# Kernel optimization log

Hardware: AMD Instinct MI355X
Metric: run time of the kernel (lower is better)

## Reference

```python
import jax, jax.numpy as jnp
import numpy as np

D = 256      # hidden_dim
NH = 8       # num_heads
DH = D // NH # head_dim = 32
K = 5        # base_kernel -> NA3D kernel (5,5,5), causal on axis 0 (time)
EPS = 1e-6


def _axis_idx(L, k, causal):
    """Per-axis NATTEN neighbor indices [L, k] and validity mask [L, k]."""
    i = jnp.arange(L)
    o = jnp.arange(k)
    if causal:
        idx = i[:, None] - (k - 1) + o[None, :]   # last k positions incl. self
        mask = idx >= 0
        idx = jnp.clip(idx, 0, L - 1)
    else:
        start = jnp.clip(i - k // 2, 0, L - k)     # window shifts at borders
        idx = start[:, None] + o[None, :]
        mask = jnp.ones((L, k), dtype=bool)
    return idx, mask


def _rmsnorm(x, w):
    return x * jax.lax.rsqrt(jnp.mean(x * x, axis=-1, keepdims=True) + EPS) * w


def _na3d(x, wq, bq, wk, bk, wv, bv, wo, bo):
    # x: [B, T, H, W, D]; neighborhood attention, causal in T.
    B, T, H, W, Dm = x.shape
    q = (x @ wq + bq).reshape(B, T, H, W, NH, DH)
    k = (x @ wk + bk).reshape(B, T, H, W, NH, DH)
    v = (x @ wv + bv).reshape(B, T, H, W, NH, DH)

    tidx, tmask = _axis_idx(T, K, True)
    hidx, _ = _axis_idx(H, K, False)
    widx, _ = _axis_idx(W, K, False)

    # Gather neighbor windows: [B, T, H, W, K, K, K, NH, DH]
    ti = tidx[:, None, None, :, None, None]
    hi = hidx[None, :, None, None, :, None]
    wi = widx[None, None, :, None, None, :]
    kn = k[:, ti, hi, wi].reshape(B, T, H, W, K ** 3, NH, DH)
    vn = v[:, ti, hi, wi].reshape(B, T, H, W, K ** 3, NH, DH)

    # Validity mask (only causal time axis masks anything): [T, H, W, K^3]
    mask = jnp.broadcast_to(tmask[:, None, None, :, None, None],
                            (T, H, W, K, K, K)).reshape(T, H, W, K ** 3)

    logits = jnp.einsum('bthwnd,bthwmnd->bthwnm', q, kn) * (DH ** -0.5)
    logits = jnp.where(mask[None, :, :, :, None, :], logits, -jnp.inf)
    attn = jax.nn.softmax(logits, axis=-1)
    out = jnp.einsum('bthwnm,bthwmnd->bthwnd', attn, vn).reshape(B, T, H, W, Dm)
    return out @ wo + bo


def setup_inputs() -> dict:
    key = jax.random.key(0)
    ks = jax.random.split(key, 14)
    w = lambda k_, shape: jax.random.normal(k_, shape, jnp.float32) * 0.02
    return {
        'x': jax.random.normal(ks[0], (1, 8, 16, 16, D), jnp.float32),
        'norm1_w': jnp.ones((D,), jnp.float32),
        'norm2_w': jnp.ones((D,), jnp.float32),
        'wq': w(ks[1], (D, D)), 'bq': jnp.zeros((D,), jnp.float32),
        'wk': w(ks[2], (D, D)), 'bk': jnp.zeros((D,), jnp.float32),
        'wv': w(ks[3], (D, D)), 'bv': jnp.zeros((D,), jnp.float32),
        'wo': w(ks[4], (D, D)), 'bo': jnp.zeros((D,), jnp.float32),
        'w1': w(ks[5], (D, 4 * D)),
        'w2': w(ks[6], (D, 4 * D)),
        'w3': w(ks[7], (4 * D, D)),
    }


def reference(x, norm1_w, norm2_w, wq, bq, wk, bk, wv, bv, wo, bo, w1, w2, w3):
    # residual NA block
    h = x + _na3d(_rmsnorm(x, norm1_w), wq, bq, wk, bk, wv, bv, wo, bo)
    # residual SwiGLU FFN block
    y = _rmsnorm(h, norm2_w)
    h = h + (jax.nn.silu(y @ w1) * (y @ w2)) @ w3
    return h
```

## Files before the change

### kernel.cpp

```cpp
#include <hip/hip_runtime.h>
#include <hip/hip_bf16.h>

typedef __attribute__((ext_vector_type(8))) __bf16 bf16x8;
typedef __attribute__((ext_vector_type(4))) __bf16 bf16x4;
typedef __attribute__((ext_vector_type(4))) short shortx4;
typedef __attribute__((ext_vector_type(4))) float f32x4;

#define D    256
#define FF   1024
#define NTOK 2048

__device__ __forceinline__ float ldf(const void* p, int i, bool isf32){
  return isf32 ? ((const float*)p)[i] : (float)(((const __bf16*)p)[i]);
}

__device__ __forceinline__ f32x4 mfma16x16x16bf16(bf16x4 a, bf16x4 b, f32x4 c){
#if __has_builtin(__builtin_amdgcn_mfma_f32_16x16x16_bf16)
  return __builtin_amdgcn_mfma_f32_16x16x16_bf16(a, b, c, 0, 0, 0);
#elif __has_builtin(__builtin_amdgcn_mfma_f32_16x16x16bf16_1k)
  return __builtin_amdgcn_mfma_f32_16x16x16bf16_1k(__builtin_bit_cast(shortx4, a),
                                                   __builtin_bit_cast(shortx4, b), c, 0, 0, 0);
#else
  asm volatile("v_mfma_f32_16x16x16_bf16 %0, %1, %2, %0" : "+v"(c) : "v"(a), "v"(b));
  return c;
#endif
}

struct MiscArgs { const void* x; const void* vec[6]; };
struct TPArgs { const void* src[7]; };

__global__ __launch_bounds__(256) void prep_kernel(MiscArgs a, TPArgs ta,
                                                   float* __restrict__ X,
                                                   float* __restrict__ VEC,
                                                   __bf16* __restrict__ WT,
                                                   __bf16* __restrict__ XN,
                                                   const unsigned int* __restrict__ tagp){
  __shared__ float tl[32][33];
  __shared__ float red[4];
  bool isf32 = (*tagp == 0x3F800000u);
  int b = blockIdx.x, tid = threadIdx.x;

  if (b < 1024){
    const void* src; int Kd, Nd, dstOff, tk, tn;
    if (b < 256){
      int mat = b >> 6, t = b & 63;
      src = ta.src[mat]; Kd = 256; Nd = 256; dstOff = mat*65536;
      tk = t >> 3; tn = t & 7;
    } else if (b < 768){
      int mat = (b - 256) >> 8, t = (b - 256) & 255;
      src = ta.src[4 + mat]; Kd = 256; Nd = 1024; dstOff = 262144 + mat*262144;
      tk = t >> 5; tn = t & 31;
    } else {
      int t = b - 768;
      src = ta.src[6]; Kd = 1024; Nd = 256; dstOff = 786432;
      tk = t >> 3; tn = t & 7;
    }
    int tx = tid & 31, ty = tid >> 5;
    int k0 = tk*32, n0 = tn*32;
    #pragma unroll
    for (int i = 0; i < 4; i++){
      int kk = ty + i*8;
      tl[kk][tx] = ldf(src, (k0 + kk)*Nd + n0 + tx, isf32);
    }
    __syncthreads();
    #pragma unroll
    for (int i = 0; i < 4; i++){
      int nn = ty + i*8;
      WT[dstOff + (n0 + nn)*Kd + k0 + tx] = (__bf16)tl[tx][nn];
    }
  } else if (b < 3072){
    int tok = b - 1024;
    int idx = tok*D + tid;
    float xv = ldf(a.x, idx, isf32);
    X[idx] = xv;
    float s = xv*xv;
    #pragma unroll
    for (int d = 32; d > 0; d >>= 1) s += __shfl_xor(s, d, 64);
    if ((tid & 63) == 0) red[tid >> 6] = s;
    __syncthreads();
    float tot = red[0]+red[1]+red[2]+red[3];
    float w = ldf(a.vec[0], tid, isf32);
    XN[idx] = (__bf16)(xv * rsqrtf(tot*(1.0f/D) + 1e-6f) * w);
  } else {
    for (int i = tid; i < 1536; i += 256)
      VEC[i] = ldf(a.vec[i >> 8], i & 255, isf32);
  }
}

__global__ __launch_bounds__(256) void rmsnorm_kernel(const float* __restrict__ x,
                                                      const float* __restrict__ w,
                                                      __bf16* __restrict__ out){
  int tok = blockIdx.x, tid = threadIdx.x;
  int idx = tok*D + tid;
  float xv = x[idx];
  float s = xv*xv;
  #pragma unroll
  for (int d = 32; d > 0; d >>= 1) s += __shfl_xor(s, d, 64);
  __shared__ float red[4];
  if ((tid & 63) == 0) red[tid >> 6] = s;
  __syncthreads();
  float tot = red[0]+red[1]+red[2]+red[3];
  out[idx] = (__bf16)(xv * rsqrtf(tot*(1.0f/D) + 1e-6f) * w[tid]);
}

typedef __bf16 ldsrow[72];

__device__ __forceinline__ void gemm_core(const __bf16* __restrict__ A,
                                          const __bf16* __restrict__ B,
                                          int K, int m0, int n0,
                                          ldsrow* As, ldsrow* Bs,
                                          f32x4 acc[2][2]){
  int tid = threadIdx.x;
  int wave = tid >> 6, lane = tid & 63;
  int wrow = wave & 1, wcol = wave >> 1;
  int q = lane >> 4, ln = lane & 15;
  for (int k0 = 0; k0 < K; k0 += 64){
    #pragma unroll
    for (int j = 0; j < 2; j++){
      int c = j*256 + tid;
      int row = c >> 3, seg = c & 7;
      *(float4*)&As[row][seg*8] = *(const float4*)&A[(m0+row)*K + k0 + seg*8];
      *(float4*)&Bs[row][seg*8] = *(const float4*)&B[(n0+row)*K + k0 + seg*8];
    }
    __syncthreads();
    #pragma unroll
    for (int ks = 0; ks < 2; ks++){
      bf16x8 a0 = *(const bf16x8*)&As[wrow*32      + ln][ks*32 + q*8];
      bf16x8 a1 = *(const bf16x8*)&As[wrow*32 + 16 + ln][ks*32 + q*8];
      bf16x8 b0 = *(const bf16x8*)&Bs[wcol*32      + ln][ks*32 + q*8];
      bf16x8 b1 = *(const bf16x8*)&Bs[wcol*32 + 16 + ln][ks*32 + q*8];
      acc[0][0] = __builtin_amdgcn_mfma_f32_16x16x32_bf16(a0, b0, acc[0][0], 0, 0, 0);
      acc[0][1] = __builtin_amdgcn_mfma_f32_16x16x32_bf16(a0, b1, acc[0][1], 0, 0, 0);
      acc[1][0] = __builtin_amdgcn_mfma_f32_16x16x32_bf16(a1, b0, acc[1][0], 0, 0, 0);
      acc[1][1] = __builtin_amdgcn_mfma_f32_16x16x32_bf16(a1, b1, acc[1][1], 0, 0, 0);
    }
    __syncthreads();
  }
}

#define GEMM_PROLOGUE \
  int tid = threadIdx.x; \
  int wave = tid >> 6, lane = tid & 63; \
  int wrow = wave & 1, wcol = wave >> 1; \
  int q = lane >> 4, ln = lane & 15; \
  (void)tid; \
  f32x4 acc[2][2]; \
  acc[0][0] = (f32x4){0,0,0,0}; acc[0][1] = (f32x4){0,0,0,0}; \
  acc[1][0] = (f32x4){0,0,0,0}; acc[1][1] = (f32x4){0,0,0,0};

__global__ __launch_bounds__(256) void qkv_kernel(const __bf16* __restrict__ xn,
                                                  const __bf16* __restrict__ WT,
                                                  const float* __restrict__ VEC,
                                                  __bf16* __restrict__ Qb,
                                                  __bf16* __restrict__ Kb,
                                                  __bf16* __restrict__ VTb){
  __shared__ __align__(16) __bf16 As[64][72];
  __shared__ __align__(16) __bf16 Bs[64][72];
  int m0 = blockIdx.x*64;
  int sel = blockIdx.y >> 2, n0 = (blockIdx.y & 3)*64;
  const __bf16* B = WT + sel*65536;
  const float* bias = VEC + 512 + sel*256;
  GEMM_PROLOGUE
  gemm_core(xn, B, D, m0, n0, As, Bs, acc);
  if (sel < 2){
    __bf16* O = (sel == 0) ? Qb : Kb;
    #pragma unroll
    for (int c = 0; c < 2; c++){
      int col = n0 + wcol*32 + c*16 + ln;
      float bv = bias[col];
      #pragma unroll
      for (int r = 0; r < 2; r++){
        #pragma unroll
        for (int i = 0; i < 4; i++){
          int m = m0 + wrow*32 + r*16 + q*4 + i;
          O[m*D + col] = (__bf16)(acc[r][c][i] + bv);
        }
      }
    }
  } else {
    #pragma unroll
    for (int c = 0; c < 2; c++){
      int col = n0 + wcol*32 + c*16 + ln;
      float bv = bias[col];
      #pragma unroll
      for (int r = 0; r < 2; r++){
        int mb = m0 + wrow*32 + r*16 + q*4;
        bf16x4 pk;
        #pragma unroll
        for (int i = 0; i < 4; i++) pk[i] = (__bf16)(acc[r][c][i] + bv);
        *(bf16x4*)&VTb[col*NTOK + mb] = pk;
      }
    }
  }
}

__global__ __launch_bounds__(256) void attn_kernel(const __bf16* __restrict__ Qb,
                                                   const __bf16* __restrict__ Kb,
                                                   const __bf16* __restrict__ VT,
                                                   __bf16* __restrict__ attn){
  int row = blockIdx.x;
  int tq = row >> 4, hq = row & 15;
  int g  = (blockIdx.y << 2) + (threadIdx.x >> 6);
  int lane = threadIdx.x & 63;
  int ln = lane & 15, qt = lane >> 4;

  int qbase = (tq << 8) + (hq << 4);
  int h0 = min(max(hq - 2, 0), 11);
  int tlo = max(tq - 4, 0);

  bf16x8 qf = *(const bf16x8*)&Qb[(qbase + ln)*D + g*32 + qt*8];

  int wstart = min(max(ln - 2, 0), 11);
  float msk[4];
  #pragma unroll
  for (int r = 0; r < 4; r++){
    int wk = qt*4 + r;
    msk[r] = (wk >= wstart && wk <= wstart + 4) ? 0.0f : -INFINITY;
  }

  const float sc = 0.17677669529663687f;
  float m_run = -INFINITY, l_run = 0.0f;
  f32x4 o0 = (f32x4){0,0,0,0}, o1 = (f32x4){0,0,0,0};
  f32x4 zero = (f32x4){0,0,0,0};

  for (int tp = tlo; tp <= tq; tp++){
    #pragma unroll
    for (int hp = 0; hp < 5; hp++){
      int kb0 = (tp << 8) + ((h0 + hp) << 4);
      bf16x8 kf = *(const bf16x8*)&Kb[(kb0 + ln)*D + g*32 + qt*8];
      f32x4 s = __builtin_amdgcn_mfma_f32_16x16x32_bf16(kf, qf, zero, 0, 0, 0);
      float sv0 = s[0]*sc + msk[0];
      float sv1 = s[1]*sc + msk[1];
      float sv2 = s[2]*sc + msk[2];
      float sv3 = s[3]*sc + msk[3];
      float tm = fmaxf(fmaxf(sv0, sv1), fmaxf(sv2, sv3));
      tm = fmaxf(tm, __shfl_xor(tm, 16, 64));
      tm = fmaxf(tm, __shfl_xor(tm, 32, 64));
      float mnew = fmaxf(m_run, tm);
      float rs = __expf(m_run - mnew);
      float p0 = __expf(sv0 - mnew), p1 = __expf(sv1 - mnew);
      float p2 = __expf(sv2 - mnew), p3 = __expf(sv3 - mnew);
      bf16x4 pa;
      pa[0] = (__bf16)p0; pa[1] = (__bf16)p1; pa[2] = (__bf16)p2; pa[3] = (__bf16)p3;
      l_run = l_run*rs + (float)pa[0] + (float)pa[1] + (float)pa[2] + (float)pa[3];
      #pragma unroll
      for (int i = 0; i < 4; i++){ o0[i] *= rs; o1[i] *= rs; }
      m_run = mnew;
      bf16x4 v0 = *(const bf16x4*)&VT[(g*32      + ln)*NTOK + kb0 + qt*4];
      bf16x4 v1 = *(const bf16x4*)&VT[(g*32 + 16 + ln)*NTOK + kb0 + qt*4];
      o0 = mfma16x16x16bf16(v0, pa, o0);
      o1 = mfma16x16x16bf16(v1, pa, o1);
    }
  }
  l_run += __shfl_xor(l_run, 16, 64);
  l_run += __shfl_xor(l_run, 32, 64);
  float linv = 1.0f / l_run;
  int obase = (qbase + ln)*D + g*32;
  bf16x4 s0, s1;
  #pragma unroll
  for (int r = 0; r < 4; r++){
    s0[r] = (__bf16)(o0[r] * linv);
    s1[r] = (__bf16)(o1[r] * linv);
  }
  *(bf16x4*)&attn[obase      + qt*4] = s0;
  *(bf16x4*)&attn[obase + 16 + qt*4] = s1;
}

__global__ __launch_bounds__(256) void oproj_kernel(const __bf16* __restrict__ A,
                                                    const __bf16* __restrict__ WoT,
                                                    const float* __restrict__ VEC,
                                                    const float* __restrict__ X,
                                                    float* __restrict__ h){
  __shared__ __align__(16) __bf16 As[64][72];
  __shared__ __align__(16) __bf16 Bs[64][72];
  int m0 = blockIdx.x*64, n0 = blockIdx.y*64;
  GEMM_PROLOGUE
  gemm_core(A, WoT, D, m0, n0, As, Bs, acc);
  #pragma unroll
  for (int c = 0; c < 2; c++){
    int col = n0 + wcol*32 + c*16 + ln;
    float bv = VEC[1280 + col];
    #pragma unroll
    for (int r = 0; r < 2; r++){
      #pragma unroll
      for (int i = 0; i < 4; i++){
        int m = m0 + wrow*32 + r*16 + q*4 + i;
        int idx = m*D + col;
        h[idx] = acc[r][c][i] + bv + X[idx];
      }
    }
  }
}

__global__ __launch_bounds__(256) void ffn1_kernel(const __bf16* __restrict__ y,
                                                   const __bf16* __restrict__ W1T,
                                                   const __bf16* __restrict__ W2T,
                                                   __bf16* __restrict__ ffh){
  __shared__ __align__(16) __bf16 As [64][72];
  __shared__ __align__(16) __bf16 B1s[64][72];
  __shared__ __align__(16) __bf16 B2s[64][72];
  int m0 = blockIdx.x*64, n0 = blockIdx.y*64;
  int tid = threadIdx.x;
  int wave = tid >> 6, lane = tid & 63;
  int wrow = wave & 1, wcol = wave >> 1;
  int q = lane >> 4, ln = lane & 15;
  f32x4 acc1[2][2], acc2[2][2];
  #pragma unroll
  for (int r = 0; r < 2; r++)
    #pragma unroll
    for (int c = 0; c < 2; c++){ acc1[r][c] = (f32x4){0,0,0,0}; acc2[r][c] = (f32x4){0,0,0,0}; }

  for (int k0 = 0; k0 < D; k0 += 64){
    #pragma unroll
    for (int j = 0; j < 2; j++){
      int c = j*256 + tid;
      int row = c >> 3, seg = c & 7;
      *(float4*)&As [row][seg*8] = *(const float4*)&y  [(m0+row)*D + k0 + seg*8];
      *(float4*)&B1s[row][seg*8] = *(const float4*)&W1T[(n0+row)*D + k0 + seg*8];
      *(float4*)&B2s[row][seg*8] = *(const float4*)&W2T[(n0+row)*D + k0 + seg*8];
    }
    __syncthreads();
    #pragma unroll
    for (int ks = 0; ks < 2; ks++){
      bf16x8 a0 = *(const bf16x8*)&As [wrow*32      + ln][ks*32 + q*8];
      bf16x8 a1 = *(const bf16x8*)&As [wrow*32 + 16 + ln][ks*32 + q*8];
      bf16x8 p0 = *(const bf16x8*)&B1s[wcol*32      + ln][ks*32 + q*8];
      bf16x8 p1 = *(const bf16x8*)&B1s[wcol*32 + 16 + ln][ks*32 + q*8];
      bf16x8 u0 = *(const bf16x8*)&B2s[wcol*32      + ln][ks*32 + q*8];
      bf16x8 u1 = *(const bf16x8*)&B2s[wcol*32 + 16 + ln][ks*32 + q*8];
      acc1[0][0] = __builtin_amdgcn_mfma_f32_16x16x32_bf16(a0, p0, acc1[0][0], 0,0,0);
      acc1[0][1] = __builtin_amdgcn_mfma_f32_16x16x32_bf16(a0, p1, acc1[0][1], 0,0,0);
      acc1[1][0] = __builtin_amdgcn_mfma_f32_16x16x32_bf16(a1, p0, acc1[1][0], 0,0,0);
      acc1[1][1] = __builtin_amdgcn_mfma_f32_16x16x32_bf16(a1, p1, acc1[1][1], 0,0,0);
      acc2[0][0] = __builtin_amdgcn_mfma_f32_16x16x32_bf16(a0, u0, acc2[0][0], 0,0,0);
      acc2[0][1] = __builtin_amdgcn_mfma_f32_16x16x32_bf16(a0, u1, acc2[0][1], 0,0,0);
      acc2[1][0] = __builtin_amdgcn_mfma_f32_16x16x32_bf16(a1, u0, acc2[1][0], 0,0,0);
      acc2[1][1] = __builtin_amdgcn_mfma_f32_16x16x32_bf16(a1, u1, acc2[1][1], 0,0,0);
    }
    __syncthreads();
  }
  #pragma unroll
  for (int c = 0; c < 2; c++){
    int col = n0 + wcol*32 + c*16 + ln;
    #pragma unroll
    for (int r = 0; r < 2; r++){
      #pragma unroll
      for (int i = 0; i < 4; i++){
        int m = m0 + wrow*32 + r*16 + q*4 + i;
        float gv = acc1[r][c][i], u = acc2[r][c][i];
        float sig = 1.0f / (1.0f + __expf(-gv));
        ffh[m*FF + col] = (__bf16)(gv * sig * u);
      }
    }
  }
}

__global__ __launch_bounds__(256) void ffn2_kernel(const __bf16* __restrict__ ffh,
                                                   const __bf16* __restrict__ W3T,
                                                   const float* __restrict__ h,
                                                   const unsigned int* __restrict__ tagp,
                                                   void* __restrict__ outp){
  __shared__ __align__(16) __bf16 As[64][72];
  __shared__ __align__(16) __bf16 Bs[64][72];
  int m0 = blockIdx.x*64, n0 = blockIdx.y*64;
  GEMM_PROLOGUE
  gemm_core(ffh, W3T, FF, m0, n0, As, Bs, acc);
  bool isf32 = (*tagp == 0x3F800000u);
  #pragma unroll
  for (int c = 0; c < 2; c++){
    int col = n0 + wcol*32 + c*16 + ln;
    #pragma unroll
    for (int r = 0; r < 2; r++){
      #pragma unroll
      for (int i = 0; i < 4; i++){
        int m = m0 + wrow*32 + r*16 + q*4 + i;
        int idx = m*D + col;
        float val = acc[r][c][i] + h[idx];
        if (isf32) ((float*)outp)[idx] = val;
        else       ((__bf16*)outp)[idx] = (__bf16)val;
      }
    }
  }
}

extern "C" void kernel_launch(void* const* d_in, const int* in_sizes, int n_in,
                              void* d_out, int out_size, void* d_ws, size_t ws_size,
                              hipStream_t stream){
  char* ws = (char*)d_ws;
  float*  X    = (float*)(ws);
  float*  VEC  = (float*)(ws + 2097152);
  __bf16* WT   = (__bf16*)(ws + 2097152 + 8192);
  __bf16* XN   = (__bf16*)(ws + 4202496);
  __bf16* Qb   = (__bf16*)(ws + 5251072);
  __bf16* Kb   = Qb + NTOK*D;
  __bf16* VTb  = Kb + NTOK*D;
  __bf16* ATT  = (__bf16*)(ws + 11542528);
  float*  Hb   = (float*)(ws + 12591104);
  __bf16* Yb   = (__bf16*)(ws + 14688256);
  __bf16* FFH  = (__bf16*)Qb;

  const unsigned int* tagp = (const unsigned int*)d_in[1];

  MiscArgs ma;
  ma.x = d_in[0];
  ma.vec[0] = d_in[1]; ma.vec[1] = d_in[2]; ma.vec[2] = d_in[4];
  ma.vec[3] = d_in[6]; ma.vec[4] = d_in[8]; ma.vec[5] = d_in[10];

  TPArgs ta;
  ta.src[0] = d_in[3];  ta.src[1] = d_in[5];  ta.src[2] = d_in[7];
  ta.src[3] = d_in[9];  ta.src[4] = d_in[11]; ta.src[5] = d_in[12];
  ta.src[6] = d_in[13];

  prep_kernel<<<3073, 256, 0, stream>>>(ma, ta, X, VEC, WT, XN, tagp);
  qkv_kernel<<<dim3(NTOK/64, 12), 256, 0, stream>>>(XN, WT, VEC, Qb, Kb, VTb);
  attn_kernel<<<dim3(128, 2), 256, 0, stream>>>(Qb, Kb, VTb, ATT);
  oproj_kernel<<<dim3(NTOK/64, 4), 256, 0, stream>>>(ATT, WT + 196608, VEC, X, Hb);
  rmsnorm_kernel<<<NTOK, 256, 0, stream>>>(Hb, VEC + 256, Yb);
  ffn1_kernel<<<dim3(NTOK/64, 16), 256, 0, stream>>>(Yb, WT + 262144, WT + 524288, FFH);
  ffn2_kernel<<<dim3(NTOK/64, 4), 256, 0, stream>>>(FFH, WT + 786432, Hb, tagp, d_out);
}
```

Baseline: 158.3 us.

## Use full-K XOR-swizzled LDS tiles in GEMM kernels to cut barriers

```diff
diff --git a/kernel.cpp b/kernel.cpp
--- a/kernel.cpp
+++ b/kernel.cpp
@@ -103,38 +103,50 @@
   out[idx] = (__bf16)(xv * rsqrtf(tot*(1.0f/D) + 1e-6f) * w[tid]);
 }
 
-typedef __bf16 ldsrow[72];
-
-__device__ __forceinline__ void gemm_core(const __bf16* __restrict__ A,
-                                          const __bf16* __restrict__ B,
-                                          int K, int m0, int n0,
-                                          ldsrow* As, ldsrow* Bs,
-                                          f32x4 acc[2][2]){
+
+__device__ __forceinline__ void stage256(const __bf16* __restrict__ src, int strideElems,
+                                         __bf16* __restrict__ lds){
   int tid = threadIdx.x;
-  int wave = tid >> 6, lane = tid & 63;
-  int wrow = wave & 1, wcol = wave >> 1;
-  int q = lane >> 4, ln = lane & 15;
-  for (int k0 = 0; k0 < K; k0 += 64){
-    #pragma unroll
-    for (int j = 0; j < 2; j++){
-      int c = j*256 + tid;
-      int row = c >> 3, seg = c & 7;
-      *(float4*)&As[row][seg*8] = *(const float4*)&A[(m0+row)*K + k0 + seg*8];
-      *(float4*)&Bs[row][seg*8] = *(const float4*)&B[(n0+row)*K + k0 + seg*8];
-    }
-    __syncthreads();
-    #pragma unroll
-    for (int ks = 0; ks < 2; ks++){
-      bf16x8 a0 = *(const bf16x8*)&As[wrow*32      + ln][ks*32 + q*8];
-      bf16x8 a1 = *(const bf16x8*)&As[wrow*32 + 16 + ln][ks*32 + q*8];
-      bf16x8 b0 = *(const bf16x8*)&Bs[wcol*32      + ln][ks*32 + q*8];
-      bf16x8 b1 = *(const bf16x8*)&Bs[wcol*32 + 16 + ln][ks*32 + q*8];
-      acc[0][0] = __builtin_amdgcn_mfma_f32_16x16x32_bf16(a0, b0, acc[0][0], 0, 0, 0);
-      acc[0][1] = __builtin_amdgcn_mfma_f32_16x16x32_bf16(a0, b1, acc[0][1], 0, 0, 0);
-      acc[1][0] = __builtin_amdgcn_mfma_f32_16x16x32_bf16(a1, b0, acc[1][0], 0, 0, 0);
-      acc[1][1] = __builtin_amdgcn_mfma_f32_16x16x32_bf16(a1, b1, acc[1][1], 0, 0, 0);
-    }
-    __syncthreads();
+  #pragma unroll
+  for (int c = 0; c < 8; c++){
+    int s = (c*256 + tid) << 4;
+    int row = s >> 9, col = s & 511;
+    *(float4*)((char*)lds + row*512 + (col ^ ((row & 7) << 4))) =
+      *(const float4*)((const char*)src + row*strideElems*2 + col);
+  }
+}
+__device__ __forceinline__ bf16x8 lrd256(const __bf16* __restrict__ lds, int row, int cb){
+  return *(const bf16x8*)((const char*)lds + row*512 + (cb ^ ((row & 7) << 4)));
+}
+
+__device__ __forceinline__ void stage128(const __bf16* __restrict__ src, int strideElems,
+                                         __bf16* __restrict__ lds){
+  int tid = threadIdx.x;
+  #pragma unroll
+  for (int c = 0; c < 4; c++){
+    int s = (c*256 + tid) << 4;
+    int row = s >> 8, col = s & 255;
+    *(float4*)((char*)lds + row*256 + (col ^ ((row & 7) << 4))) =
+      *(const float4*)((const char*)src + row*strideElems*2 + col);
+  }
+}
+__device__ __forceinline__ bf16x8 lrd128(const __bf16* __restrict__ lds, int row, int cb){
+  return *(const bf16x8*)((const char*)lds + row*256 + (cb ^ ((row & 7) << 4)));
+}
+
+__device__ __forceinline__ void mfma256(const __bf16* __restrict__ As, const __bf16* __restrict__ Bs,
+                                        f32x4 acc[2][2], int wrow, int wcol, int q, int ln){
+  #pragma unroll
+  for (int ks = 0; ks < 8; ks++){
+    int cb = ks*64 + q*16;
+    bf16x8 a0 = lrd256(As, wrow*32      + ln, cb);
+    bf16x8 a1 = lrd256(As, wrow*32 + 16 + ln, cb);
+    bf16x8 b0 = lrd256(Bs, wcol*32      + ln, cb);
+    bf16x8 b1 = lrd256(Bs, wcol*32 + 16 + ln, cb);
+    acc[0][0] = __builtin_amdgcn_mfma_f32_16x16x32_bf16(a0, b0, acc[0][0], 0, 0, 0);
+    acc[0][1] = __builtin_amdgcn_mfma_f32_16x16x32_bf16(a0, b1, acc[0][1], 0, 0, 0);
+    acc[1][0] = __builtin_amdgcn_mfma_f32_16x16x32_bf16(a1, b0, acc[1][0], 0, 0, 0);
+    acc[1][1] = __builtin_amdgcn_mfma_f32_16x16x32_bf16(a1, b1, acc[1][1], 0, 0, 0);
   }
 }
 
@@ -154,14 +166,17 @@
                                                   __bf16* __restrict__ Qb,
                                                   __bf16* __restrict__ Kb,
                                                   __bf16* __restrict__ VTb){
-  __shared__ __align__(16) __bf16 As[64][72];
-  __shared__ __align__(16) __bf16 Bs[64][72];
+  __shared__ __align__(16) __bf16 As[64][256];
+  __shared__ __align__(16) __bf16 Bs[64][256];
   int m0 = blockIdx.x*64;
   int sel = blockIdx.y >> 2, n0 = (blockIdx.y & 3)*64;
   const __bf16* B = WT + sel*65536;
   const float* bias = VEC + 512 + sel*256;
   GEMM_PROLOGUE
-  gemm_core(xn, B, D, m0, n0, As, Bs, acc);
+  stage256(xn + m0*D, D, &As[0][0]);
+  stage256(B  + n0*D, D, &Bs[0][0]);
+  __syncthreads();
+  mfma256(&As[0][0], &Bs[0][0], acc, wrow, wcol, q, ln);
   if (sel < 2){
     __bf16* O = (sel == 0) ? Qb : Kb;
     #pragma unroll
@@ -271,11 +286,14 @@
                                                     const float* __restrict__ VEC,
                                                     const float* __restrict__ X,
                                                     float* __restrict__ h){
-  __shared__ __align__(16) __bf16 As[64][72];
-  __shared__ __align__(16) __bf16 Bs[64][72];
+  __shared__ __align__(16) __bf16 As[64][256];
+  __shared__ __align__(16) __bf16 Bs[64][256];
   int m0 = blockIdx.x*64, n0 = blockIdx.y*64;
   GEMM_PROLOGUE
-  gemm_core(A, WoT, D, m0, n0, As, Bs, acc);
+  stage256(A   + m0*D, D, &As[0][0]);
+  stage256(WoT + n0*D, D, &Bs[0][0]);
+  __syncthreads();
+  mfma256(&As[0][0], &Bs[0][0], acc, wrow, wcol, q, ln);
   #pragma unroll
   for (int c = 0; c < 2; c++){
     int col = n0 + wcol*32 + c*16 + ln;
@@ -296,9 +314,9 @@
                                                    const __bf16* __restrict__ W1T,
                                                    const __bf16* __restrict__ W2T,
                                                    __bf16* __restrict__ ffh){
-  __shared__ __align__(16) __bf16 As [64][72];
-  __shared__ __align__(16) __bf16 B1s[64][72];
-  __shared__ __align__(16) __bf16 B2s[64][72];
+  __shared__ __align__(16) __bf16 As [64][128];
+  __shared__ __align__(16) __bf16 B1s[64][128];
+  __shared__ __align__(16) __bf16 B2s[64][128];
   int m0 = blockIdx.x*64, n0 = blockIdx.y*64;
   int tid = threadIdx.x;
   int wave = tid >> 6, lane = tid & 63;
@@ -310,24 +328,22 @@
     #pragma unroll
     for (int c = 0; c < 2; c++){ acc1[r][c] = (f32x4){0,0,0,0}; acc2[r][c] = (f32x4){0,0,0,0}; }
 
-  for (int k0 = 0; k0 < D; k0 += 64){
-    #pragma unroll
-    for (int j = 0; j < 2; j++){
-      int c = j*256 + tid;
-      int row = c >> 3, seg = c & 7;
-      *(float4*)&As [row][seg*8] = *(const float4*)&y  [(m0+row)*D + k0 + seg*8];
-      *(float4*)&B1s[row][seg*8] = *(const float4*)&W1T[(n0+row)*D + k0 + seg*8];
-      *(float4*)&B2s[row][seg*8] = *(const float4*)&W2T[(n0+row)*D + k0 + seg*8];
-    }
+  #pragma unroll
+  for (int k0 = 0; k0 < D; k0 += 128){
+    if (k0) __syncthreads();
+    stage128(y   + m0*D + k0, D, &As [0][0]);
+    stage128(W1T + n0*D + k0, D, &B1s[0][0]);
+    stage128(W2T + n0*D + k0, D, &B2s[0][0]);
     __syncthreads();
     #pragma unroll
-    for (int ks = 0; ks < 2; ks++){
-      bf16x8 a0 = *(const bf16x8*)&As [wrow*32      + ln][ks*32 + q*8];
-      bf16x8 a1 = *(const bf16x8*)&As [wrow*32 + 16 + ln][ks*32 + q*8];
-      bf16x8 p0 = *(const bf16x8*)&B1s[wcol*32      + ln][ks*32 + q*8];
-      bf16x8 p1 = *(const bf16x8*)&B1s[wcol*32 + 16 + ln][ks*32 + q*8];
-      bf16x8 u0 = *(const bf16x8*)&B2s[wcol*32      + ln][ks*32 + q*8];
-      bf16x8 u1 = *(const bf16x8*)&B2s[wcol*32 + 16 + ln][ks*32 + q*8];
+    for (int ks = 0; ks < 4; ks++){
+      int cb = ks*64 + q*16;
+      bf16x8 a0 = lrd128(&As [0][0], wrow*32      + ln, cb);
+      bf16x8 a1 = lrd128(&As [0][0], wrow*32 + 16 + ln, cb);
+      bf16x8 p0 = lrd128(&B1s[0][0], wcol*32      + ln, cb);
+      bf16x8 p1 = lrd128(&B1s[0][0], wcol*32 + 16 + ln, cb);
+      bf16x8 u0 = lrd128(&B2s[0][0], wcol*32      + ln, cb);
+      bf16x8 u1 = lrd128(&B2s[0][0], wcol*32 + 16 + ln, cb);
       acc1[0][0] = __builtin_amdgcn_mfma_f32_16x16x32_bf16(a0, p0, acc1[0][0], 0,0,0);
       acc1[0][1] = __builtin_amdgcn_mfma_f32_16x16x32_bf16(a0, p1, acc1[0][1], 0,0,0);
       acc1[1][0] = __builtin_amdgcn_mfma_f32_16x16x32_bf16(a1, p0, acc1[1][0], 0,0,0);
@@ -337,7 +353,6 @@
       acc2[1][0] = __builtin_amdgcn_mfma_f32_16x16x32_bf16(a1, u0, acc2[1][0], 0,0,0);
       acc2[1][1] = __builtin_amdgcn_mfma_f32_16x16x32_bf16(a1, u1, acc2[1][1], 0,0,0);
     }
-    __syncthreads();
   }
   #pragma unroll
   for (int c = 0; c < 2; c++){
@@ -360,11 +375,18 @@
                                                    const float* __restrict__ h,
                                                    const unsigned int* __restrict__ tagp,
                                                    void* __restrict__ outp){
-  __shared__ __align__(16) __bf16 As[64][72];
-  __shared__ __align__(16) __bf16 Bs[64][72];
+  __shared__ __align__(16) __bf16 As[64][256];
+  __shared__ __align__(16) __bf16 Bs[64][256];
   int m0 = blockIdx.x*64, n0 = blockIdx.y*64;
   GEMM_PROLOGUE
-  gemm_core(ffh, W3T, FF, m0, n0, As, Bs, acc);
+  #pragma unroll
+  for (int k0 = 0; k0 < FF; k0 += 256){
+    if (k0) __syncthreads();
+    stage256(ffh + m0*FF + k0, FF, &As[0][0]);
+    stage256(W3T + n0*FF + k0, FF, &Bs[0][0]);
+    __syncthreads();
+    mfma256(&As[0][0], &Bs[0][0], acc, wrow, wcol, q, ln);
+  }
   bool isf32 = (*tagp == 0x3F800000u);
   #pragma unroll
   for (int c = 0; c < 2; c++){
```

After: 135.1 us. 1.17x faster.
